# Kernel tuning notes

Measured on AMD Instinct MI355X. Metric: run time of the kernel, lower is better.

## Reference

```python
import jax, jax.numpy as jnp
import numpy as np

EPS = 1e-5

def group_norm(x, gamma, beta, groups):
    # x: (B, C, D, H, W)
    B, C = x.shape[0], x.shape[1]
    xr = x.reshape(B, groups, C // groups, -1)
    mean = xr.mean(axis=(2, 3), keepdims=True)
    var = xr.var(axis=(2, 3), keepdims=True)
    xn = ((xr - mean) * jax.lax.rsqrt(var + EPS)).reshape(x.shape)
    return xn * gamma[None, :, None, None, None] + beta[None, :, None, None, None]

def setup_inputs() -> dict:
    key = jax.random.key(0)
    ks = jax.random.split(key, 8)
    B, Ccls = 2, 32
    D = H = W = 64
    s = 0.05
    return {
        "x": jax.random.normal(ks[0], (B, 768, 8, 8, 8), jnp.float32),
        "out": jax.random.normal(ks[1], (B, 48, D, H, W), jnp.float32),
        "task_encoding": jax.random.normal(ks[2], (Ccls, 256, 1, 1, 1), jnp.float32),
        "gn1_g": jnp.ones((768,), jnp.float32),
        "gn1_b": jnp.zeros((768,), jnp.float32),
        "gap_w": jax.random.normal(ks[3], (256, 768), jnp.float32) * s,
        "gap_b": jnp.zeros((256,), jnp.float32),
        "ctrl_w": jax.random.normal(ks[4], (153, 512), jnp.float32) * s,
        "ctrl_b": jnp.zeros((153,), jnp.float32),
        "gn2_g": jnp.ones((48,), jnp.float32),
        "gn2_b": jnp.zeros((48,), jnp.float32),
        "pre_w": jax.random.normal(ks[5], (8, 48), jnp.float32) * s,
        "pre_b": jnp.zeros((8,), jnp.float32),
    }

def reference(x, out, task_encoding, gn1_g, gn1_b, gap_w, gap_b, ctrl_w, ctrl_b,
              gn2_g, gn2_b, pre_w, pre_b):
    B = x.shape[0]
    Ccls = task_encoding.shape[0]
    # GAP branch: GroupNorm(16,768) -> ReLU -> global avg pool -> 1x1x1 conv 768->256
    h = jax.nn.relu(group_norm(x, gn1_g, gn1_b, 16))
    pooled = h.mean(axis=(2, 3, 4))                       # (B, 768)
    x_feat = pooled @ gap_w.T + gap_b                     # (B, 256)
    # Controller: per (batch, class) params from concat(x_feat, task_encoding)
    te = task_encoding.reshape(Ccls, -1)                  # (Ccls, 256)
    params = (jnp.einsum('pf,bf->bp', ctrl_w[:, :256], x_feat)[:, None, :]
              + jnp.einsum('pf,cf->cp', ctrl_w[:, 256:], te)[None, :, :]
              + ctrl_b)                                   # (B, Ccls, 153)
    w1 = params[..., 0:64].reshape(B, Ccls, 8, 8)
    w2 = params[..., 64:128].reshape(B, Ccls, 8, 8)
    w3 = params[..., 128:136].reshape(B, Ccls, 1, 8)
    b1 = params[..., 136:144]
    b2 = params[..., 144:152]
    b3 = params[..., 152:153]
    # precls branch: GroupNorm(16,48) -> ReLU -> 1x1x1 conv 48->8
    g = jax.nn.relu(group_norm(out, gn2_g, gn2_b, 16))
    h0 = jnp.einsum('oc,bcdhw->bodhw', pre_w, g) + pre_b[None, :, None, None, None]
    # Dynamic per-class head: 8->8->8->1 pointwise MLP with ReLU between layers
    t = jax.nn.relu(jnp.einsum('bcij,bjdhw->bcidhw', w1, h0) + b1[..., None, None, None])
    t = jax.nn.relu(jnp.einsum('bcij,bcjdhw->bcidhw', w2, t) + b2[..., None, None, None])
    logits = jnp.einsum('bcij,bcjdhw->bcidhw', w3, t) + b3[..., None, None, None]
    # (B, Ccls, 1, D, H, W) -> (B, Ccls, D, H, W)
    return logits[:, :, 0]
```

## Files before the change

### kernel.cpp

```cpp
#include <hip/hip_runtime.h>

constexpr int NCLS = 32;

constexpr int WS_POOL = 64;
constexpr int WS_XF  = 1600;
constexpr int WS_PAR = 2112;
constexpr int WS_P2  = 11904;

typedef float f2 __attribute__((ext_vector_type(2)));

__device__ __forceinline__ float wred(float v) {
#pragma unroll
  for (int off = 32; off > 0; off >>= 1) v += __shfl_down(v, off, 64);
  return v;
}

__device__ __forceinline__ f2 pfma(float w, f2 v, f2 a) {
  return __builtin_elementwise_fma((f2)w, v, a);
}
__device__ __forceinline__ f2 paff(f2 v, float sc, float sh) {
  return __builtin_elementwise_fma(v, (f2)sc, (f2)sh);
}
__device__ __forceinline__ f2 prelu(f2 a) {
  return __builtin_elementwise_max(a, (f2)0.f);
}

__global__ void k1_stats(const float* __restrict__ x, const float* __restrict__ oin,
                         const float* __restrict__ g1, const float* __restrict__ b1,
                         float* __restrict__ ws) {
  int t = threadIdx.x;
  int wid = t >> 6, lane = t & 63;
  __shared__ float red[8];
  if (blockIdx.x < 768) {
    int blk = blockIdx.x;
    const float4* p = reinterpret_cast<const float4*>(oin + (size_t)blk * 32768);
    float s = 0.f, s2 = 0.f;
#pragma unroll
    for (int k = 0; k < 32; ++k) {
      float4 v = p[k * 256 + t];
      s  += v.x + v.y + v.z + v.w;
      s2 += v.x*v.x + v.y*v.y + v.z*v.z + v.w*v.w;
    }
    s = wred(s); s2 = wred(s2);
    if (lane == 0) { red[wid*2] = s; red[wid*2+1] = s2; }
    __syncthreads();
    if (t == 0) {
      ws[WS_P2 + blk*2]   = red[0]+red[2]+red[4]+red[6];
      ws[WS_P2 + blk*2+1] = red[1]+red[3]+red[5]+red[7];
    }
  } else {
    int g = blockIdx.x - 768;
    __shared__ float mstat[2];
    const float4* p = reinterpret_cast<const float4*>(x + g * 24576);
    float s = 0.f, s2 = 0.f;
#pragma unroll
    for (int k = 0; k < 24; ++k) {
      float4 v = p[k * 256 + t];
      s  += v.x + v.y + v.z + v.w;
      s2 += v.x*v.x + v.y*v.y + v.z*v.z + v.w*v.w;
    }
    s = wred(s); s2 = wred(s2);
    if (lane == 0) { red[wid*2] = s; red[wid*2+1] = s2; }
    __syncthreads();
    if (t == 0) {
      float S  = red[0]+red[2]+red[4]+red[6];
      float S2 = red[1]+red[3]+red[5]+red[7];
      float mean = S * (1.f/24576.f);
      float var  = S2 * (1.f/24576.f) - mean*mean;
      mstat[0] = mean; mstat[1] = rsqrtf(var + 1e-5f);
    }
    __syncthreads();
    float mean = mstat[0], rstd = mstat[1];
#pragma unroll
    for (int k = 0; k < 12; ++k) {
      int i = k*4 + wid;
      int c = (g & 15) * 48 + i;
      float sc = rstd * g1[c];
      float sh = b1[c] - mean * sc;
      const float* q = x + g * 24576 + i * 512;
      float acc = 0.f;
#pragma unroll
      for (int j = 0; j < 8; ++j)
        acc += fmaxf(fmaf(q[lane + j*64], sc, sh), 0.f);
      acc = wred(acc);
      if (lane == 0) ws[WS_POOL + (g >> 4) * 768 + c] = acc * (1.f/512.f);
    }
  }
}

__global__ void k2_xfeat(const float* __restrict__ gapw, const float* __restrict__ gapb,
                         float* __restrict__ ws) {
  int wid = threadIdx.x >> 6, lane = threadIdx.x & 63;
  int idx = blockIdx.x * 4 + wid;
  int b = idx >> 8, o = idx & 255;
  const float* pw = gapw + o * 768;
  const float* pp = ws + WS_POOL + b * 768;
  float s = 0.f;
#pragma unroll
  for (int i = 0; i < 12; ++i) {
    int cc = lane + i*64;
    s += pw[cc] * pp[cc];
  }
  s = wred(s);
  if (lane == 0) ws[WS_XF + idx] = s + gapb[o];
}

__global__ void k3_params(const float* __restrict__ cw, const float* __restrict__ cb,
                          const float* __restrict__ te, float* __restrict__ ws) {
  int wid = threadIdx.x >> 6, lane = threadIdx.x & 63;
  int e = blockIdx.x * 4 + wid;
  int b = e / (NCLS * 153);
  int r = e % (NCLS * 153);
  int c = r / 153, p = r % 153;
  const float* w  = cw + p * 512;
  const float* xf = ws + WS_XF + b * 256;
  const float* tv = te + c * 256;
  float s = 0.f;
#pragma unroll
  for (int i = 0; i < 4; ++i) {
    int f = lane + i*64;
    s += w[f] * xf[f] + w[256 + f] * tv[f];
  }
  s = wred(s);
  if (lane == 0) ws[WS_PAR + e] = s + cb[p];
}

__global__ __launch_bounds__(256) void k4_main(const float* __restrict__ oin,
                                               const float* __restrict__ prew,
                                               const float* __restrict__ preb,
                                               const float* __restrict__ g2,
                                               const float* __restrict__ b2,
                                               const float* __restrict__ ws,
                                               float* __restrict__ out) {
  __shared__ __align__(16) float prewT[384];
  __shared__ float2 ssl[48];
  __shared__ float ms[64];
  int t = threadIdx.x;
  int b    = blockIdx.x >> 7;
  int tile = blockIdx.x & 127;

  if (t < 32) {
    float S = 0.f, S2 = 0.f;
#pragma unroll
    for (int k = 0; k < 24; ++k) {
      S  += ws[WS_P2 + (t*24 + k)*2];
      S2 += ws[WS_P2 + (t*24 + k)*2 + 1];
    }
    float mean = S * (1.f/786432.f);
    float var  = S2 * (1.f/786432.f) - mean*mean;
    ms[t*2] = mean; ms[t*2+1] = rsqrtf(var + 1e-5f);
  }
  if (t < 128) {
#pragma unroll
    for (int k = 0; k < 3; ++k) {
      int i = t + k*128;
      prewT[(i % 48) * 8 + (i / 48)] = prew[i];
    }
  }
  __syncthreads();
  if (t < 48) {
    int grp = (b << 4) + t / 3;
    float mean = ms[grp*2], rstd = ms[grp*2+1];
    float sc = rstd * g2[t];
    ssl[t] = make_float2(sc, b2[t] - mean * sc);
  }
  __syncthreads();

  const float4* ip4 = reinterpret_cast<const float4*>(oin)
                      + (size_t)b * 48 * 65536 + tile*512 + t;
  const float4* pT4 = reinterpret_cast<const float4*>(prewT);
  f2 h0[8][4];
#pragma unroll
  for (int o = 0; o < 8; ++o) {
    float pb = preb[o];
#pragma unroll
    for (int p = 0; p < 4; ++p) h0[o][p] = (f2)pb;
  }
#pragma unroll 8
  for (int c = 0; c < 48; ++c) {
    float4 va = ip4[(size_t)c * 65536];
    float4 vb = ip4[(size_t)c * 65536 + 256];
    float2 ss = ssl[c];
    f2 g[4];
    g[0] = prelu(paff((f2){va.x, va.y}, ss.x, ss.y));
    g[1] = prelu(paff((f2){va.z, va.w}, ss.x, ss.y));
    g[2] = prelu(paff((f2){vb.x, vb.y}, ss.x, ss.y));
    g[3] = prelu(paff((f2){vb.z, vb.w}, ss.x, ss.y));
    float4 w0 = pT4[c*2], w1 = pT4[c*2+1];
    float wv[8] = {w0.x, w0.y, w0.z, w0.w, w1.x, w1.y, w1.z, w1.w};
#pragma unroll
    for (int o = 0; o < 8; ++o)
#pragma unroll
      for (int p = 0; p < 4; ++p) h0[o][p] = pfma(wv[o], g[p], h0[o][p]);
  }

  const float* __restrict__ Wb = ws + WS_PAR + (size_t)b * NCLS * 153;
  float4* op4 = reinterpret_cast<float4*>(out)
                + (size_t)b * NCLS * 65536 + tile*512 + t;
#pragma unroll 1
  for (int cls = 0; cls < NCLS; ++cls) {
    const float* Wc = Wb + cls * 153;
    f2 t1[8][4];
#pragma unroll
    for (int i = 0; i < 8; ++i) {
      float bi = Wc[136 + i];
      f2 a[4];
#pragma unroll
      for (int p = 0; p < 4; ++p) a[p] = (f2)bi;
#pragma unroll
      for (int j = 0; j < 8; ++j) {
        float w = Wc[i*8 + j];
#pragma unroll
        for (int p = 0; p < 4; ++p) a[p] = pfma(w, h0[j][p], a[p]);
      }
#pragma unroll
      for (int p = 0; p < 4; ++p) t1[i][p] = prelu(a[p]);
    }
    float b3v = Wc[152];
    f2 lg[4];
#pragma unroll
    for (int p = 0; p < 4; ++p) lg[p] = (f2)b3v;
#pragma unroll
    for (int i = 0; i < 8; ++i) {
      float bi = Wc[144 + i];
      f2 a[4];
#pragma unroll
      for (int p = 0; p < 4; ++p) a[p] = (f2)bi;
#pragma unroll
      for (int j = 0; j < 8; ++j) {
        float w = Wc[64 + i*8 + j];
#pragma unroll
        for (int p = 0; p < 4; ++p) a[p] = pfma(w, t1[j][p], a[p]);
      }
      float w3 = Wc[128 + i];
#pragma unroll
      for (int p = 0; p < 4; ++p) {
        a[p] = prelu(a[p]);
        lg[p] = pfma(w3, a[p], lg[p]);
      }
    }
    op4[(size_t)cls * 65536]       = make_float4(lg[0].x, lg[0].y, lg[1].x, lg[1].y);
    op4[(size_t)cls * 65536 + 256] = make_float4(lg[2].x, lg[2].y, lg[3].x, lg[3].y);
  }
}

extern "C" void kernel_launch(void* const* d_in, const int* in_sizes, int n_in,
                              void* d_out, int out_size, void* d_ws, size_t ws_size,
                              hipStream_t stream) {
  const float* x    = (const float*)d_in[0];
  const float* oin  = (const float*)d_in[1];
  const float* te   = (const float*)d_in[2];
  const float* g1   = (const float*)d_in[3];
  const float* b1   = (const float*)d_in[4];
  const float* gapw = (const float*)d_in[5];
  const float* gapb = (const float*)d_in[6];
  const float* cw   = (const float*)d_in[7];
  const float* cb   = (const float*)d_in[8];
  const float* g2   = (const float*)d_in[9];
  const float* b2   = (const float*)d_in[10];
  const float* prew = (const float*)d_in[11];
  const float* preb = (const float*)d_in[12];
  float* ws  = (float*)d_ws;
  float* out = (float*)d_out;

  hipLaunchKernelGGL(k1_stats,  dim3(800),  dim3(256), 0, stream, x, oin, g1, b1, ws);
  hipLaunchKernelGGL(k2_xfeat,  dim3(128),  dim3(256), 0, stream, gapw, gapb, ws);
  hipLaunchKernelGGL(k3_params, dim3(2448), dim3(256), 0, stream, cw, cb, te, ws);
  hipLaunchKernelGGL(k4_main,   dim3(256),  dim3(256), 0, stream, oin, prew, preb, g2, b2, ws, out);
}
```

Baseline: 305.3 us.

## Split class loop across two blocks and stage layer-1 weights in LDS

The main kernel's grid doubles so that each block handles half of the 32 classes for its spatial tile, which raises the number of blocks available to fill the GPU. The cost is that each block recomputes the 48->8 pre-conv and rereads the input tile, doubling reads of the large input. The first-layer weights and biases for the block's 16 classes are now staged in shared memory and loaded as float4 vectors, instead of being read as scalars from global memory. A scheduling barrier is added after those weight loads.

```diff
diff --git a/kernel.cpp b/kernel.cpp
--- a/kernel.cpp
+++ b/kernel.cpp
@@ -132,12 +132,15 @@
                                                const float* __restrict__ b2,
                                                const float* __restrict__ ws,
                                                float* __restrict__ out) {
+  __shared__ __align__(16) float Wl[16 * 80];
   __shared__ __align__(16) float prewT[384];
   __shared__ float2 ssl[48];
   __shared__ float ms[64];
   int t = threadIdx.x;
-  int b    = blockIdx.x >> 7;
-  int tile = blockIdx.x & 127;
+  int b    = blockIdx.x >> 8;
+  int rem  = blockIdx.x & 255;
+  int tile = rem >> 1;
+  int cls0 = (rem & 1) << 4;
 
   if (t < 32) {
     float S = 0.f, S2 = 0.f;
@@ -156,6 +159,15 @@
       int i = t + k*128;
       prewT[(i % 48) * 8 + (i / 48)] = prew[i];
     }
+  }
+  {
+    const float* wsrc = ws + WS_PAR + (size_t)(b * NCLS + cls0) * 153;
+#pragma unroll 4
+    for (int cc = 0; cc < 16; ++cc)
+      if (t < 72) {
+        int src = (t < 64) ? t : (136 + t - 64);
+        Wl[cc*80 + t] = wsrc[cc*153 + src];
+      }
   }
   __syncthreads();
   if (t < 48) {
@@ -194,28 +206,36 @@
       for (int p = 0; p < 4; ++p) h0[o][p] = pfma(wv[o], g[p], h0[o][p]);
   }
 
-  const float* __restrict__ Wb = ws + WS_PAR + (size_t)b * NCLS * 153;
+  const float* __restrict__ Wb = ws + WS_PAR + (size_t)(b * NCLS + cls0) * 153;
   float4* op4 = reinterpret_cast<float4*>(out)
-                + (size_t)b * NCLS * 65536 + tile*512 + t;
+                + (size_t)(b * NCLS + cls0) * 65536 + tile*512 + t;
 #pragma unroll 1
-  for (int cls = 0; cls < NCLS; ++cls) {
+  for (int cls = 0; cls < 16; ++cls) {
+    const float4* WA = reinterpret_cast<const float4*>(Wl + cls * 80);
+    float4 w1r[16];
+#pragma unroll
+    for (int k = 0; k < 16; ++k) w1r[k] = WA[k];
+    float4 b1q0 = WA[16], b1q1 = WA[17];
+    __builtin_amdgcn_sched_barrier(0);
+    float b1arr[8] = {b1q0.x,b1q0.y,b1q0.z,b1q0.w,b1q1.x,b1q1.y,b1q1.z,b1q1.w};
+
+    f2 t1[8][4];
+#pragma unroll
+    for (int i = 0; i < 8; ++i) {
+      float4 wa = w1r[i*2], wb = w1r[i*2+1];
+      float wv[8] = {wa.x, wa.y, wa.z, wa.w, wb.x, wb.y, wb.z, wb.w};
+      f2 a[4];
+#pragma unroll
+      for (int p = 0; p < 4; ++p) a[p] = (f2)b1arr[i];
+#pragma unroll
+      for (int j = 0; j < 8; ++j)
+#pragma unroll
+        for (int p = 0; p < 4; ++p) a[p] = pfma(wv[j], h0[j][p], a[p]);
+#pragma unroll
+      for (int p = 0; p < 4; ++p) t1[i][p] = prelu(a[p]);
+    }
+
     const float* Wc = Wb + cls * 153;
-    f2 t1[8][4];
-#pragma unroll
-    for (int i = 0; i < 8; ++i) {
-      float bi = Wc[136 + i];
-      f2 a[4];
-#pragma unroll
-      for (int p = 0; p < 4; ++p) a[p] = (f2)bi;
-#pragma unroll
-      for (int j = 0; j < 8; ++j) {
-        float w = Wc[i*8 + j];
-#pragma unroll
-        for (int p = 0; p < 4; ++p) a[p] = pfma(w, h0[j][p], a[p]);
-      }
-#pragma unroll
-      for (int p = 0; p < 4; ++p) t1[i][p] = prelu(a[p]);
-    }
     float b3v = Wc[152];
     f2 lg[4];
 #pragma unroll
@@ -266,5 +286,5 @@
   hipLaunchKernelGGL(k1_stats,  dim3(800),  dim3(256), 0, stream, x, oin, g1, b1, ws);
   hipLaunchKernelGGL(k2_xfeat,  dim3(128),  dim3(256), 0, stream, gapw, gapb, ws);
   hipLaunchKernelGGL(k3_params, dim3(2448), dim3(256), 0, stream, cw, cb, te, ws);
-  hipLaunchKernelGGL(k4_main,   dim3(256),  dim3(256), 0, stream, oin, prew, preb, g2, b2, ws, out);
-}
+  hipLaunchKernelGGL(k4_main,   dim3(512),  dim3(256), 0, stream, oin, prew, preb, g2, b2, ws, out);
+}
```

New measurement: 276.1 us. 9.6% less time.
